# Kernel tuning notes

Measured on AMD Instinct MI355X. Metric: run time of the kernel, lower is better.

Reference implementation:

```python
import jax, jax.numpy as jnp
import numpy as np

B, V, E, D_IN, D_OUT = 8, 10000, 160000, 128, 128
BN_EPS = 1e-5


def setup_inputs() -> dict:
    key = jax.random.key(0)
    ks = jax.random.split(key, 8)
    X = jax.random.normal(ks[0], (B, V, D_IN), dtype=jnp.float32)
    edge_attr = jax.random.normal(ks[1], (B, E), dtype=jnp.float32)
    W_node = jax.random.normal(ks[2], (D_OUT, D_IN), dtype=jnp.float32) * (1.0 / np.sqrt(D_IN))
    W_edge = jax.random.normal(ks[3], (D_OUT, 1), dtype=jnp.float32)
    W_self = jax.random.normal(ks[4], (D_OUT, D_IN), dtype=jnp.float32) * (1.0 / np.sqrt(D_IN))
    b_self = jax.random.normal(ks[5], (D_OUT,), dtype=jnp.float32) * 0.01
    gamma = jnp.ones((D_OUT,), dtype=jnp.float32)
    beta = jnp.zeros((D_OUT,), dtype=jnp.float32)
    edge_index = jax.random.randint(ks[6], (E, 2), 0, V, dtype=jnp.int32)
    return {"X": X, "edge_attr": edge_attr, "W_node": W_node, "W_edge": W_edge,
            "W_self": W_self, "b_self": b_self, "gamma": gamma, "beta": beta,
            "edge_index": edge_index}


def reference(X, edge_attr, W_node, W_edge, W_self, b_self, gamma, beta, edge_index):
    src = edge_index[:, 0]  # [E]
    dst = edge_index[:, 1]  # [E]
    # self-loop linear
    H = jnp.einsum('bvf,of->bvo', X, W_self) + b_self  # [B,V,D_OUT]
    # fused gather -> per-edge message -> scatter-add
    msg = jnp.einsum('bef,of->beo', X[:, src, :], W_node)  # [B,E,D_OUT]
    msg = msg + edge_attr[:, :, None] * W_edge[:, 0][None, None, :]
    aggregated = jnp.zeros_like(H).at[:, dst, :].add(msg)
    H = H + aggregated
    # BatchNorm1d over channel dim (training mode, biased variance over B*V)
    mean = jnp.mean(H, axis=(0, 1))
    var = jnp.var(H, axis=(0, 1))
    Hn = (H - mean) * jax.lax.rsqrt(var + BN_EPS) * gamma + beta
    return jax.nn.relu(Hn)
```

## Files before the change

kernel.cpp:

```cpp
#include <hip/hip_runtime.h>

#define B_ 8
#define V_ 10000
#define E_ 160000
#define DIN 128
#define DOUT 128
#define M_ (B_*V_)
#define NINV (1.0f/80000.0f)
#define BN_EPS 1e-5f

#define GEMM_BLOCKS 625
#define CAP 64

#define WS_CNT     0
#define WS_SUM     10000
#define WS_SUMSQ   10128
#define WS_ZERO_UNITS 10256
#define WS_S       10256
#define WS_SSRC    90256
#define WS_EAS     730256
#define WS_HH      730256
#define WS_WPK     5850256
#define WS_XH      5866640
#define WS_AH      10986640

typedef __attribute__((ext_vector_type(2))) _Float16 half2_t;
typedef __attribute__((ext_vector_type(4))) _Float16 half4_t;
typedef __attribute__((ext_vector_type(8))) _Float16 half8_t;
typedef __attribute__((ext_vector_type(4))) float f32x4;

__device__ inline half2_t i2h(unsigned i) {
    half2_t h; __builtin_memcpy(&h, &i, 4); return h;
}
__device__ inline unsigned h2i(half2_t h) {
    unsigned i; __builtin_memcpy(&i, &h, 4); return i;
}

__global__ __launch_bounds__(256) void prep_kernel(
    const float* __restrict__ X, _Float16* __restrict__ Xh,
    const float* __restrict__ Wself, const float* __restrict__ Wnode,
    _Float16* __restrict__ Wpk,
    const int* __restrict__ EI, const float* __restrict__ EA,
    int* __restrict__ cnt, int* __restrict__ ssrc, float* __restrict__ EAs)
{
    const int blk = blockIdx.x;
    const int t = threadIdx.x;
    if (blk < 10000) {
        int idx = blk * 256 + t;
        float4 v = ((const float4*)X)[idx];
        half4_t o = { (_Float16)v.x, (_Float16)v.y, (_Float16)v.z, (_Float16)v.w };
        ((half4_t*)Xh)[idx] = o;
    } else if (blk < 10016) {
        int g = (blk - 10000) * 256 + t;
        int pair = g >> 6;
        int lane = g & 63;
        int ks = pair >> 3;
        int nt = pair & 7;
        int o = nt * 16 + (lane & 15);
        int k = ks * 32 + (lane >> 4) * 8;
        const float* wsrc = (k < 128) ? (Wself + o * 128 + k)
                                      : (Wnode + o * 128 + (k - 128));
        _Float16* dst = Wpk + ((size_t)pair * 64 + lane) * 8;
#pragma unroll
        for (int j = 0; j < 8; ++j) dst[j] = (_Float16)wsrc[j];
    } else {
        int e = (blk - 10016) * 256 + t;
        int src = EI[2 * e];
        int dst = EI[2 * e + 1];
        int slot = atomicAdd(&cnt[dst], 1);
        if (slot < CAP) {
            int p = dst * CAP + slot;
            ssrc[p] = src;
            float4 v0, v1;
            v0.x = EA[0 * E_ + e]; v0.y = EA[1 * E_ + e];
            v0.z = EA[2 * E_ + e]; v0.w = EA[3 * E_ + e];
            v1.x = EA[4 * E_ + e]; v1.y = EA[5 * E_ + e];
            v1.z = EA[6 * E_ + e]; v1.w = EA[7 * E_ + e];
            *(float4*)(EAs + (size_t)p * 8) = v0;
            *(float4*)(EAs + (size_t)p * 8 + 4) = v1;
        }
    }
}

__global__ __launch_bounds__(256) void gather_kernel(
    const _Float16* __restrict__ Xh, const float* __restrict__ EAs,
    const int* __restrict__ cnt, const int* __restrict__ ssrc,
    _Float16* __restrict__ Ah, float* __restrict__ S)
{
    const int b = blockIdx.x & 7;
    const int dblk = blockIdx.x >> 3;
    const int w = threadIdx.x >> 6;
    const int lane = threadIdx.x & 63;
    const int q = lane >> 4;
    const int sl = lane & 15;
    const int d = dblk * 4 + w;
    const int wid = b * V_ + d;
    const int deg = min(cnt[d], CAP);
    const int k0 = d * CAP;
    const _Float16* Xb = Xh + (size_t)b * V_ * DIN + sl * 8;
    half2_t a0 = (half2_t)0, a1 = (half2_t)0, a2 = (half2_t)0, a3 = (half2_t)0;
    float ea = 0.0f;
    {
        int msrc = 0;
        if (lane < deg) {
            msrc = ssrc[k0 + lane];
            ea = EAs[(size_t)(k0 + lane) * 8 + b];
        }
        int j = 0;
        for (; j + 16 <= deg; j += 16) {
#pragma unroll
            for (int u = 0; u < 4; ++u) {
                int s = __shfl(msrc, j + u * 4 + q);
                uint4 v = *(const uint4*)(Xb + (size_t)s * DIN);
                a0 += i2h(v.x); a1 += i2h(v.y); a2 += i2h(v.z); a3 += i2h(v.w);
            }
        }
        for (; j + 4 <= deg; j += 4) {
            int s = __shfl(msrc, j + q);
            uint4 v = *(const uint4*)(Xb + (size_t)s * DIN);
            a0 += i2h(v.x); a1 += i2h(v.y); a2 += i2h(v.z); a3 += i2h(v.w);
        }
        if (j < deg) {
            int s = __shfl(msrc, j + q);
            if (j + q < deg) {
                uint4 v = *(const uint4*)(Xb + (size_t)s * DIN);
                a0 += i2h(v.x); a1 += i2h(v.y); a2 += i2h(v.z); a3 += i2h(v.w);
            }
        }
    }
#pragma unroll
    for (int off = 32; off >= 16; off >>= 1) {
        a0 += i2h(__shfl_down(h2i(a0), off));
        a1 += i2h(__shfl_down(h2i(a1), off));
        a2 += i2h(__shfl_down(h2i(a2), off));
        a3 += i2h(__shfl_down(h2i(a3), off));
    }
    for (int off = 32; off; off >>= 1) ea += __shfl_down(ea, off);
    if (lane == 0) S[wid] = ea;
    if (lane < 16) {
        uint4 o;
        o.x = h2i(a0); o.y = h2i(a1); o.z = h2i(a2); o.w = h2i(a3);
        *(uint4*)(Ah + (size_t)wid * DIN + sl * 8) = o;
    }
}

__global__ __launch_bounds__(256) void gemm_stats_kernel(
    const _Float16* __restrict__ Xh, const _Float16* __restrict__ Ah,
    const _Float16* __restrict__ Wpk, const float* __restrict__ S,
    const float* __restrict__ bself, const float* __restrict__ wedge,
    _Float16* __restrict__ Hh, float* __restrict__ gsum,
    float* __restrict__ gsumsq)
{
    __shared__ _Float16 wlds[32768];
    __shared__ float cs[128];
    __shared__ float css[128];
    const int t = threadIdx.x;
    const int wave = t >> 6;
    const int lane = t & 63;
    const int quad = lane >> 4;
    const int ln = lane & 15;
    const int rowbase = blockIdx.x * 128 + wave * 32;
    const int m0 = rowbase + ln;
    const int m1 = rowbase + 16 + ln;

#pragma unroll
    for (int i = 0; i < 16; ++i) {
        int chunk = wave * 16 + i;
        __builtin_amdgcn_global_load_lds(
            (const __attribute__((address_space(1))) void*)
                ((const char*)Wpk + (size_t)chunk * 1024 + lane * 16),
            (__attribute__((address_space(3))) void*)
                ((char*)wlds + (size_t)chunk * 1024),
            16, 0, 0);
    }

    if (t < 128) { cs[t] = 0.0f; css[t] = 0.0f; }

    f32x4 acc[2][8];
#pragma unroll
    for (int mt = 0; mt < 2; ++mt)
#pragma unroll
        for (int nt = 0; nt < 8; ++nt) acc[mt][nt] = (f32x4){0.f, 0.f, 0.f, 0.f};

    const _Float16* X0 = Xh + (size_t)m0 * DIN + quad * 8;
    const _Float16* X1 = Xh + (size_t)m1 * DIN + quad * 8;
    const _Float16* A0 = Ah + (size_t)m0 * DIN + quad * 8;
    const _Float16* A1 = Ah + (size_t)m1 * DIN + quad * 8;

    half8_t afr[2][8];
#pragma unroll
    for (int ks = 0; ks < 4; ++ks) {
        afr[0][ks]     = *(const half8_t*)(X0 + ks * 32);
        afr[1][ks]     = *(const half8_t*)(X1 + ks * 32);
        afr[0][4 + ks] = *(const half8_t*)(A0 + ks * 32);
        afr[1][4 + ks] = *(const half8_t*)(A1 + ks * 32);
    }

    __syncthreads();

#pragma unroll
    for (int ks = 0; ks < 8; ++ks) {
#pragma unroll
        for (int nt = 0; nt < 8; ++nt) {
            half8_t bfr = *(const half8_t*)(wlds + (size_t)(ks * 8 + nt) * 512 + lane * 8);
            acc[0][nt] = __builtin_amdgcn_mfma_f32_16x16x32_f16(afr[0][ks], bfr, acc[0][nt], 0, 0, 0);
            acc[1][nt] = __builtin_amdgcn_mfma_f32_16x16x32_f16(afr[1][ks], bfr, acc[1][nt], 0, 0, 0);
        }
    }

    float bs[8], we[8];
#pragma unroll
    for (int nt = 0; nt < 8; ++nt) {
        int c = nt * 16 + ln;
        bs[nt] = bself[c];
        we[nt] = wedge[c];
    }
    float psum[8], psq[8];
#pragma unroll
    for (int nt = 0; nt < 8; ++nt) { psum[nt] = 0.0f; psq[nt] = 0.0f; }

#pragma unroll
    for (int mt = 0; mt < 2; ++mt) {
        const int rbase = rowbase + mt * 16 + quad * 4;
        float sv[4];
#pragma unroll
        for (int r = 0; r < 4; ++r) sv[r] = S[rbase + r];
#pragma unroll
        for (int r = 0; r < 4; ++r) {
            _Float16* Hr = Hh + (size_t)(rbase + r) * DOUT + ln;
#pragma unroll
            for (int nt = 0; nt < 8; ++nt) {
                float h = acc[mt][nt][r] + bs[nt] + sv[r] * we[nt];
                Hr[nt * 16] = (_Float16)h;
                psum[nt] += h;
                psq[nt] += h * h;
            }
        }
    }
#pragma unroll
    for (int nt = 0; nt < 8; ++nt) {
        psum[nt] += __shfl_down(psum[nt], 32);
        psum[nt] += __shfl_down(psum[nt], 16);
        psq[nt] += __shfl_down(psq[nt], 32);
        psq[nt] += __shfl_down(psq[nt], 16);
    }
    __syncthreads();
    if (lane < 16) {
#pragma unroll
        for (int nt = 0; nt < 8; ++nt) {
            atomicAdd(&cs[nt * 16 + ln], psum[nt]);
            atomicAdd(&css[nt * 16 + ln], psq[nt]);
        }
    }
    __syncthreads();
    if (t < 128) atomicAdd(&gsum[t], cs[t]);
    else atomicAdd(&gsumsq[t - 128], css[t - 128]);
}

__global__ __launch_bounds__(256) void norm_relu_kernel(
    const _Float16* __restrict__ Hh, float* __restrict__ H,
    const float* __restrict__ gsum, const float* __restrict__ gsumsq,
    const float* __restrict__ gamma, const float* __restrict__ beta)
{
    const int total = M_ * DOUT / 8;
    for (int idx = blockIdx.x * 256 + threadIdx.x; idx < total;
         idx += gridDim.x * 256) {
        int o8 = (idx & 15) * 8;
        float4 s0 = *(const float4*)(gsum + o8);
        float4 s1 = *(const float4*)(gsum + o8 + 4);
        float4 q0 = *(const float4*)(gsumsq + o8);
        float4 q1 = *(const float4*)(gsumsq + o8 + 4);
        float4 g0 = *(const float4*)(gamma + o8);
        float4 g1 = *(const float4*)(gamma + o8 + 4);
        float4 b0 = *(const float4*)(beta + o8);
        float4 b1 = *(const float4*)(beta + o8 + 4);
        float sc[8], sh[8];
        float sv[8] = {s0.x, s0.y, s0.z, s0.w, s1.x, s1.y, s1.z, s1.w};
        float qv[8] = {q0.x, q0.y, q0.z, q0.w, q1.x, q1.y, q1.z, q1.w};
        float gv[8] = {g0.x, g0.y, g0.z, g0.w, g1.x, g1.y, g1.z, g1.w};
        float bv[8] = {b0.x, b0.y, b0.z, b0.w, b1.x, b1.y, b1.z, b1.w};
#pragma unroll
        for (int j = 0; j < 8; ++j) {
            float mean = sv[j] * NINV;
            float rstd = rsqrtf(qv[j] * NINV - mean * mean + BN_EPS);
            sc[j] = gv[j] * rstd;
            sh[j] = bv[j] - mean * sc[j];
        }
        half8_t hv = ((const half8_t*)Hh)[idx];
        float4 o0, o1;
        o0.x = fmaxf((float)hv[0] * sc[0] + sh[0], 0.0f);
        o0.y = fmaxf((float)hv[1] * sc[1] + sh[1], 0.0f);
        o0.z = fmaxf((float)hv[2] * sc[2] + sh[2], 0.0f);
        o0.w = fmaxf((float)hv[3] * sc[3] + sh[3], 0.0f);
        o1.x = fmaxf((float)hv[4] * sc[4] + sh[4], 0.0f);
        o1.y = fmaxf((float)hv[5] * sc[5] + sh[5], 0.0f);
        o1.z = fmaxf((float)hv[6] * sc[6] + sh[6], 0.0f);
        o1.w = fmaxf((float)hv[7] * sc[7] + sh[7], 0.0f);
        ((float4*)H)[idx * 2]     = o0;
        ((float4*)H)[idx * 2 + 1] = o1;
    }
}

extern "C" void kernel_launch(void* const* d_in, const int* in_sizes, int n_in,
                              void* d_out, int out_size, void* d_ws, size_t ws_size,
                              hipStream_t stream)
{
    const float* X      = (const float*)d_in[0];
    const float* EA     = (const float*)d_in[1];
    const float* Wnode  = (const float*)d_in[2];
    const float* Wedge  = (const float*)d_in[3];
    const float* Wself  = (const float*)d_in[4];
    const float* bself  = (const float*)d_in[5];
    const float* gamma  = (const float*)d_in[6];
    const float* beta   = (const float*)d_in[7];
    const int*   EI     = (const int*)d_in[8];

    int*   wsI    = (int*)d_ws;
    float* wsF    = (float*)d_ws;
    int*   cnt    = wsI + WS_CNT;
    float* gsum   = wsF + WS_SUM;
    float* gsumsq = wsF + WS_SUMSQ;
    float* S      = wsF + WS_S;
    int*   ssrc   = wsI + WS_SSRC;
    float* EAs    = wsF + WS_EAS;
    _Float16* Hh  = (_Float16*)(wsI + WS_HH);
    _Float16* Wpk = (_Float16*)(wsI + WS_WPK);
    _Float16* Xh  = (_Float16*)(wsI + WS_XH);
    _Float16* Ah  = (_Float16*)(wsI + WS_AH);
    float* H      = (float*)d_out;

    hipMemsetAsync(d_ws, 0, (size_t)WS_ZERO_UNITS * 4, stream);

    prep_kernel<<<10641, 256, 0, stream>>>(X, Xh, Wself, Wnode, Wpk, EI, EA,
                                           cnt, ssrc, EAs);

    gather_kernel<<<M_ / 4, 256, 0, stream>>>(Xh, EAs, cnt, ssrc, Ah, S);

    gemm_stats_kernel<<<GEMM_BLOCKS, 256, 0, stream>>>(Xh, Ah, Wpk, S, bself,
                                                       Wedge, Hh, gsum, gsumsq);

    norm_relu_kernel<<<2048, 256, 0, stream>>>(Hh, H, gsum, gsumsq, gamma, beta);
}
```

Baseline: 198.1 us.

## Fuse neighbor gather into GEMM kernel with LDS-staged aggregates and streamed weights

Removes the separate gather kernel and instead has each GEMM wave gather and sum neighbor features for its 32 rows, staging the aggregate in swizzled LDS before the MFMA loop. Weights are streamed into a smaller LDS buffer in four stages, and block IDs are remapped for XCD locality. This avoids writing and re-reading the aggregate matrix and the per-row edge sum through global memory, and saves one launch. In exchange, the gather runs in only 625 blocks with rows processed serially per wave, which cuts the latency-hiding parallelism the standalone gather had.

```diff
diff --git a/kernel.cpp b/kernel.cpp
--- a/kernel.cpp
+++ b/kernel.cpp
@@ -16,13 +16,11 @@
 #define WS_SUM     10000
 #define WS_SUMSQ   10128
 #define WS_ZERO_UNITS 10256
-#define WS_S       10256
-#define WS_SSRC    90256
-#define WS_EAS     730256
-#define WS_HH      730256
-#define WS_WPK     5850256
-#define WS_XH      5866640
-#define WS_AH      10986640
+#define WS_SSRC    10256
+#define WS_EAS     650256
+#define WS_WPK     5770256
+#define WS_XH      5786640
+#define WS_HH      10906640
 
 typedef __attribute__((ext_vector_type(2))) _Float16 half2_t;
 typedef __attribute__((ext_vector_type(4))) _Float16 half4_t;
@@ -82,129 +80,158 @@
     }
 }
 
-__global__ __launch_bounds__(256) void gather_kernel(
-    const _Float16* __restrict__ Xh, const float* __restrict__ EAs,
-    const int* __restrict__ cnt, const int* __restrict__ ssrc,
-    _Float16* __restrict__ Ah, float* __restrict__ S)
+__global__ __launch_bounds__(256, 3) void gemm_fused_kernel(
+    const _Float16* __restrict__ Xh, const _Float16* __restrict__ Wpk,
+    const float* __restrict__ EAs, const int* __restrict__ cnt,
+    const int* __restrict__ ssrc, const float* __restrict__ bself,
+    const float* __restrict__ wedge, _Float16* __restrict__ Hh,
+    float* __restrict__ gsum, float* __restrict__ gsumsq)
 {
-    const int b = blockIdx.x & 7;
-    const int dblk = blockIdx.x >> 3;
-    const int w = threadIdx.x >> 6;
-    const int lane = threadIdx.x & 63;
-    const int q = lane >> 4;
-    const int sl = lane & 15;
-    const int d = dblk * 4 + w;
-    const int wid = b * V_ + d;
-    const int deg = min(cnt[d], CAP);
-    const int k0 = d * CAP;
-    const _Float16* Xb = Xh + (size_t)b * V_ * DIN + sl * 8;
-    half2_t a0 = (half2_t)0, a1 = (half2_t)0, a2 = (half2_t)0, a3 = (half2_t)0;
-    float ea = 0.0f;
-    {
-        int msrc = 0;
-        if (lane < deg) {
-            msrc = ssrc[k0 + lane];
-            ea = EAs[(size_t)(k0 + lane) * 8 + b];
-        }
-        int j = 0;
-        for (; j + 16 <= deg; j += 16) {
-#pragma unroll
-            for (int u = 0; u < 4; ++u) {
-                int s = __shfl(msrc, j + u * 4 + q);
-                uint4 v = *(const uint4*)(Xb + (size_t)s * DIN);
-                a0 += i2h(v.x); a1 += i2h(v.y); a2 += i2h(v.z); a3 += i2h(v.w);
-            }
-        }
-        for (; j + 4 <= deg; j += 4) {
-            int s = __shfl(msrc, j + q);
-            uint4 v = *(const uint4*)(Xb + (size_t)s * DIN);
-            a0 += i2h(v.x); a1 += i2h(v.y); a2 += i2h(v.z); a3 += i2h(v.w);
-        }
-        if (j < deg) {
-            int s = __shfl(msrc, j + q);
-            if (j + q < deg) {
-                uint4 v = *(const uint4*)(Xb + (size_t)s * DIN);
-                a0 += i2h(v.x); a1 += i2h(v.y); a2 += i2h(v.z); a3 += i2h(v.w);
-            }
-        }
-    }
-#pragma unroll
-    for (int off = 32; off >= 16; off >>= 1) {
-        a0 += i2h(__shfl_down(h2i(a0), off));
-        a1 += i2h(__shfl_down(h2i(a1), off));
-        a2 += i2h(__shfl_down(h2i(a2), off));
-        a3 += i2h(__shfl_down(h2i(a3), off));
-    }
-    for (int off = 32; off; off >>= 1) ea += __shfl_down(ea, off);
-    if (lane == 0) S[wid] = ea;
-    if (lane < 16) {
-        uint4 o;
-        o.x = h2i(a0); o.y = h2i(a1); o.z = h2i(a2); o.w = h2i(a3);
-        *(uint4*)(Ah + (size_t)wid * DIN + sl * 8) = o;
-    }
-}
-
-__global__ __launch_bounds__(256) void gemm_stats_kernel(
-    const _Float16* __restrict__ Xh, const _Float16* __restrict__ Ah,
-    const _Float16* __restrict__ Wpk, const float* __restrict__ S,
-    const float* __restrict__ bself, const float* __restrict__ wedge,
-    _Float16* __restrict__ Hh, float* __restrict__ gsum,
-    float* __restrict__ gsumsq)
-{
-    __shared__ _Float16 wlds[32768];
-    __shared__ float cs[128];
-    __shared__ float css[128];
+    __shared__ _Float16 wlds[8192];
+    __shared__ _Float16 agg[16384];
+    float* cs  = (float*)agg;
+    float* css = ((float*)agg) + 128;
+
     const int t = threadIdx.x;
+    const int orig = blockIdx.x;
+    const int xcd = orig & 7, off = orig >> 3;
+    const int qq = GEMM_BLOCKS >> 3, rr = GEMM_BLOCKS & 7;
+    const int bid = (xcd < rr ? xcd * (qq + 1)
+                              : rr * (qq + 1) + (xcd - rr) * qq) + off;
+
     const int wave = t >> 6;
     const int lane = t & 63;
     const int quad = lane >> 4;
     const int ln = lane & 15;
-    const int rowbase = blockIdx.x * 128 + wave * 32;
-    const int m0 = rowbase + ln;
-    const int m1 = rowbase + 16 + ln;
-
-#pragma unroll
-    for (int i = 0; i < 16; ++i) {
-        int chunk = wave * 16 + i;
+    const int rowbase = bid * 128 + wave * 32;
+
+#pragma unroll
+    for (int i = 0; i < 4; ++i) {
+        int lc = wave * 4 + i;
         __builtin_amdgcn_global_load_lds(
             (const __attribute__((address_space(1))) void*)
-                ((const char*)Wpk + (size_t)chunk * 1024 + lane * 16),
+                ((const char*)Wpk + (size_t)lc * 1024 + lane * 16),
             (__attribute__((address_space(3))) void*)
-                ((char*)wlds + (size_t)chunk * 1024),
+                ((char*)wlds + (size_t)lc * 1024),
             16, 0, 0);
     }
 
-    if (t < 128) { cs[t] = 0.0f; css[t] = 0.0f; }
-
-    f32x4 acc[2][8];
-#pragma unroll
-    for (int mt = 0; mt < 2; ++mt)
-#pragma unroll
-        for (int nt = 0; nt < 8; ++nt) acc[mt][nt] = (f32x4){0.f, 0.f, 0.f, 0.f};
-
+    float sv[2][4];
+    for (int r = 0; r < 32; ++r) {
+        int lrow = wave * 32 + r;
+        int m = bid * 128 + lrow;
+        int b = m / V_;
+        int d = m - b * V_;
+        int deg = min(cnt[d], CAP);
+        int k0 = d * CAP;
+        const _Float16* Xb = Xh + (size_t)b * V_ * DIN + ln * 8;
+        half2_t a0 = (half2_t)0, a1 = (half2_t)0, a2 = (half2_t)0, a3 = (half2_t)0;
+        int msrc = 0; float ea = 0.0f;
+        if (lane < deg) {
+            msrc = ssrc[k0 + lane];
+            ea = EAs[(size_t)(k0 + lane) * 8 + b];
+        }
+        int j = 0;
+        for (; j + 16 <= deg; j += 16) {
+#pragma unroll
+            for (int u = 0; u < 4; ++u) {
+                int s = __shfl(msrc, j + u * 4 + quad);
+                uint4 v = *(const uint4*)(Xb + (size_t)s * DIN);
+                a0 += i2h(v.x); a1 += i2h(v.y); a2 += i2h(v.z); a3 += i2h(v.w);
+            }
+        }
+        for (; j + 4 <= deg; j += 4) {
+            int s = __shfl(msrc, j + quad);
+            uint4 v = *(const uint4*)(Xb + (size_t)s * DIN);
+            a0 += i2h(v.x); a1 += i2h(v.y); a2 += i2h(v.z); a3 += i2h(v.w);
+        }
+        if (j < deg) {
+            int s = __shfl(msrc, j + quad);
+            if (j + quad < deg) {
+                uint4 v = *(const uint4*)(Xb + (size_t)s * DIN);
+                a0 += i2h(v.x); a1 += i2h(v.y); a2 += i2h(v.z); a3 += i2h(v.w);
+            }
+        }
+#pragma unroll
+        for (int off2 = 32; off2 >= 16; off2 >>= 1) {
+            a0 += i2h(__shfl_down(h2i(a0), off2));
+            a1 += i2h(__shfl_down(h2i(a1), off2));
+            a2 += i2h(__shfl_down(h2i(a2), off2));
+            a3 += i2h(__shfl_down(h2i(a3), off2));
+        }
+        for (int off2 = 32; off2; off2 >>= 1) ea += __shfl_down(ea, off2);
+        float ea_r = __shfl(ea, 0);
+#pragma unroll
+        for (int mt = 0; mt < 2; ++mt)
+#pragma unroll
+            for (int r2 = 0; r2 < 4; ++r2)
+                if (r == mt * 16 + quad * 4 + r2) sv[mt][r2] = ea_r;
+        if (lane < 16) {
+            uint4 o; o.x = h2i(a0); o.y = h2i(a1); o.z = h2i(a2); o.w = h2i(a3);
+            int slot = lrow * 16 + (ln ^ (lrow & 7));
+            *(uint4*)((char*)agg + (size_t)slot * 16) = o;
+        }
+    }
+
+    half8_t agr0[4], agr1[4];
+    {
+        const int R0 = wave * 32 + ln;
+        const int R1 = R0 + 16;
+#pragma unroll
+        for (int ks2 = 0; ks2 < 4; ++ks2) {
+            int sl0 = R0 * 16 + ((ks2 * 4 + quad) ^ (R0 & 7));
+            int sl1 = R1 * 16 + ((ks2 * 4 + quad) ^ (R1 & 7));
+            agr0[ks2] = *(const half8_t*)((const char*)agg + (size_t)sl0 * 16);
+            agr1[ks2] = *(const half8_t*)((const char*)agg + (size_t)sl1 * 16);
+        }
+    }
+
+    const int m0 = rowbase + ln, m1 = rowbase + 16 + ln;
     const _Float16* X0 = Xh + (size_t)m0 * DIN + quad * 8;
     const _Float16* X1 = Xh + (size_t)m1 * DIN + quad * 8;
-    const _Float16* A0 = Ah + (size_t)m0 * DIN + quad * 8;
-    const _Float16* A1 = Ah + (size_t)m1 * DIN + quad * 8;
-
-    half8_t afr[2][8];
+    half8_t afr0[4], afr1[4];
 #pragma unroll
     for (int ks = 0; ks < 4; ++ks) {
-        afr[0][ks]     = *(const half8_t*)(X0 + ks * 32);
-        afr[1][ks]     = *(const half8_t*)(X1 + ks * 32);
-        afr[0][4 + ks] = *(const half8_t*)(A0 + ks * 32);
-        afr[1][4 + ks] = *(const half8_t*)(A1 + ks * 32);
-    }
+        afr0[ks] = *(const half8_t*)(X0 + ks * 32);
+        afr1[ks] = *(const half8_t*)(X1 + ks * 32);
+    }
+
+    f32x4 acc[2][8];
+#pragma unroll
+    for (int mt = 0; mt < 2; ++mt)
+#pragma unroll
+        for (int nt = 0; nt < 8; ++nt) acc[mt][nt] = (f32x4){0.f, 0.f, 0.f, 0.f};
 
     __syncthreads();
-
-#pragma unroll
-    for (int ks = 0; ks < 8; ++ks) {
-#pragma unroll
-        for (int nt = 0; nt < 8; ++nt) {
-            half8_t bfr = *(const half8_t*)(wlds + (size_t)(ks * 8 + nt) * 512 + lane * 8);
-            acc[0][nt] = __builtin_amdgcn_mfma_f32_16x16x32_f16(afr[0][ks], bfr, acc[0][nt], 0, 0, 0);
-            acc[1][nt] = __builtin_amdgcn_mfma_f32_16x16x32_f16(afr[1][ks], bfr, acc[1][nt], 0, 0, 0);
+    if (t < 128) { cs[t] = 0.0f; css[t] = 0.0f; }
+
+#pragma unroll
+    for (int s = 0; s < 4; ++s) {
+#pragma unroll
+        for (int ksl = 0; ksl < 2; ++ksl) {
+            const int kg = s * 2 + ksl;
+            half8_t af0 = (kg < 4) ? afr0[kg] : agr0[kg - 4];
+            half8_t af1 = (kg < 4) ? afr1[kg] : agr1[kg - 4];
+#pragma unroll
+            for (int nt = 0; nt < 8; ++nt) {
+                half8_t bfr = *(const half8_t*)(wlds + (size_t)(ksl * 8 + nt) * 512 + lane * 8);
+                acc[0][nt] = __builtin_amdgcn_mfma_f32_16x16x32_f16(af0, bfr, acc[0][nt], 0, 0, 0);
+                acc[1][nt] = __builtin_amdgcn_mfma_f32_16x16x32_f16(af1, bfr, acc[1][nt], 0, 0, 0);
+            }
+        }
+        if (s < 3) {
+            __syncthreads();
+#pragma unroll
+            for (int i = 0; i < 4; ++i) {
+                int lc = wave * 4 + i;
+                __builtin_amdgcn_global_load_lds(
+                    (const __attribute__((address_space(1))) void*)
+                        ((const char*)Wpk + (size_t)((s + 1) * 16 + lc) * 1024 + lane * 16),
+                    (__attribute__((address_space(3))) void*)
+                        ((char*)wlds + (size_t)lc * 1024),
+                    16, 0, 0);
+            }
+            __syncthreads();
         }
     }
 
@@ -221,16 +248,13 @@
 
 #pragma unroll
     for (int mt = 0; mt < 2; ++mt) {
-        const int rbase = rowbase + mt * 16 + quad * 4;
-        float sv[4];
-#pragma unroll
-        for (int r = 0; r < 4; ++r) sv[r] = S[rbase + r];
-#pragma unroll
-        for (int r = 0; r < 4; ++r) {
-            _Float16* Hr = Hh + (size_t)(rbase + r) * DOUT + ln;
+        const int rbl = wave * 32 + mt * 16 + quad * 4;
+#pragma unroll
+        for (int r2 = 0; r2 < 4; ++r2) {
+            _Float16* Hr = Hh + (size_t)(bid * 128 + rbl + r2) * DOUT + ln;
 #pragma unroll
             for (int nt = 0; nt < 8; ++nt) {
-                float h = acc[mt][nt][r] + bs[nt] + sv[r] * we[nt];
+                float h = acc[mt][nt][r2] + bs[nt] + sv[mt][r2] * we[nt];
                 Hr[nt * 16] = (_Float16)h;
                 psum[nt] += h;
                 psq[nt] += h * h;
@@ -241,8 +265,8 @@
     for (int nt = 0; nt < 8; ++nt) {
         psum[nt] += __shfl_down(psum[nt], 32);
         psum[nt] += __shfl_down(psum[nt], 16);
-        psq[nt] += __shfl_down(psq[nt], 32);
-        psq[nt] += __shfl_down(psq[nt], 16);
+        psq[nt]  += __shfl_down(psq[nt], 32);
+        psq[nt]  += __shfl_down(psq[nt], 16);
     }
     __syncthreads();
     if (lane < 16) {
@@ -275,13 +299,13 @@
         float4 b0 = *(const float4*)(beta + o8);
         float4 b1 = *(const float4*)(beta + o8 + 4);
         float sc[8], sh[8];
-        float sv[8] = {s0.x, s0.y, s0.z, s0.w, s1.x, s1.y, s1.z, s1.w};
+        float svv[8] = {s0.x, s0.y, s0.z, s0.w, s1.x, s1.y, s1.z, s1.w};
         float qv[8] = {q0.x, q0.y, q0.z, q0.w, q1.x, q1.y, q1.z, q1.w};
         float gv[8] = {g0.x, g0.y, g0.z, g0.w, g1.x, g1.y, g1.z, g1.w};
         float bv[8] = {b0.x, b0.y, b0.z, b0.w, b1.x, b1.y, b1.z, b1.w};
 #pragma unroll
         for (int j = 0; j < 8; ++j) {
-            float mean = sv[j] * NINV;
+            float mean = svv[j] * NINV;
             float rstd = rsqrtf(qv[j] * NINV - mean * mean + BN_EPS);
             sc[j] = gv[j] * rstd;
             sh[j] = bv[j] - mean * sc[j];
@@ -320,13 +344,11 @@
     int*   cnt    = wsI + WS_CNT;
     float* gsum   = wsF + WS_SUM;
     float* gsumsq = wsF + WS_SUMSQ;
-    float* S      = wsF + WS_S;
     int*   ssrc   = wsI + WS_SSRC;
     float* EAs    = wsF + WS_EAS;
-    _Float16* Hh  = (_Float16*)(wsI + WS_HH);
     _Float16* Wpk = (_Float16*)(wsI + WS_WPK);
     _Float16* Xh  = (_Float16*)(wsI + WS_XH);
-    _Float16* Ah  = (_Float16*)(wsI + WS_AH);
+    _Float16* Hh  = (_Float16*)(wsI + WS_HH);
     float* H      = (float*)d_out;
 
     hipMemsetAsync(d_ws, 0, (size_t)WS_ZERO_UNITS * 4, stream);
@@ -334,10 +356,9 @@
     prep_kernel<<<10641, 256, 0, stream>>>(X, Xh, Wself, Wnode, Wpk, EI, EA,
                                            cnt, ssrc, EAs);
 
-    gather_kernel<<<M_ / 4, 256, 0, stream>>>(Xh, EAs, cnt, ssrc, Ah, S);
-
-    gemm_stats_kernel<<<GEMM_BLOCKS, 256, 0, stream>>>(Xh, Ah, Wpk, S, bself,
-                                                       Wedge, Hh, gsum, gsumsq);
+    gemm_fused_kernel<<<GEMM_BLOCKS, 256, 0, stream>>>(Xh, Wpk, EAs, cnt, ssrc,
+                                                       bself, Wedge, Hh,
+                                                       gsum, gsumsq);
 
     norm_relu_kernel<<<2048, 256, 0, stream>>>(Hh, H, gsum, gsumsq, gamma, beta);
 }
```

New measurement: 216.2 us. 9.2% more time.

## Split GEMM waves across output columns with register-resident weights, drop LDS staging

Applied to the files above, without the earlier changes.

The GEMM+stats kernel now gives each wave a 32-column slice of the output for all 128 rows of the block. Weights are loaded straight into registers instead of being staged through 64KB of LDS. Per-block stat reduction through shared memory is replaced by direct global atomics, and launch bounds request 2 blocks per SM. This removes the LDS footprint and barriers, but every wave now re-reads the full A tile (X and aggregated rows) from global/L2, the global atomic count rises, and register pressure grows.

```diff
diff --git a/kernel.cpp b/kernel.cpp
--- a/kernel.cpp
+++ b/kernel.cpp
@@ -144,117 +144,94 @@
     }
 }
 
-__global__ __launch_bounds__(256) void gemm_stats_kernel(
+__global__ __launch_bounds__(256, 2) void gemm_stats_kernel(
     const _Float16* __restrict__ Xh, const _Float16* __restrict__ Ah,
     const _Float16* __restrict__ Wpk, const float* __restrict__ S,
     const float* __restrict__ bself, const float* __restrict__ wedge,
     _Float16* __restrict__ Hh, float* __restrict__ gsum,
     float* __restrict__ gsumsq)
 {
-    __shared__ _Float16 wlds[32768];
-    __shared__ float cs[128];
-    __shared__ float css[128];
     const int t = threadIdx.x;
     const int wave = t >> 6;
     const int lane = t & 63;
     const int quad = lane >> 4;
     const int ln = lane & 15;
-    const int rowbase = blockIdx.x * 128 + wave * 32;
-    const int m0 = rowbase + ln;
-    const int m1 = rowbase + 16 + ln;
-
-#pragma unroll
-    for (int i = 0; i < 16; ++i) {
-        int chunk = wave * 16 + i;
-        __builtin_amdgcn_global_load_lds(
-            (const __attribute__((address_space(1))) void*)
-                ((const char*)Wpk + (size_t)chunk * 1024 + lane * 16),
-            (__attribute__((address_space(3))) void*)
-                ((char*)wlds + (size_t)chunk * 1024),
-            16, 0, 0);
-    }
-
-    if (t < 128) { cs[t] = 0.0f; css[t] = 0.0f; }
-
-    f32x4 acc[2][8];
-#pragma unroll
-    for (int mt = 0; mt < 2; ++mt)
-#pragma unroll
-        for (int nt = 0; nt < 8; ++nt) acc[mt][nt] = (f32x4){0.f, 0.f, 0.f, 0.f};
-
-    const _Float16* X0 = Xh + (size_t)m0 * DIN + quad * 8;
-    const _Float16* X1 = Xh + (size_t)m1 * DIN + quad * 8;
-    const _Float16* A0 = Ah + (size_t)m0 * DIN + quad * 8;
-    const _Float16* A1 = Ah + (size_t)m1 * DIN + quad * 8;
-
-    half8_t afr[2][8];
-#pragma unroll
-    for (int ks = 0; ks < 4; ++ks) {
-        afr[0][ks]     = *(const half8_t*)(X0 + ks * 32);
-        afr[1][ks]     = *(const half8_t*)(X1 + ks * 32);
-        afr[0][4 + ks] = *(const half8_t*)(A0 + ks * 32);
-        afr[1][4 + ks] = *(const half8_t*)(A1 + ks * 32);
-    }
-
-    __syncthreads();
+    const int bid = blockIdx.x;
+    const int rowbase = bid * 128;
+
+    half8_t bfr[8][2];
+#pragma unroll
+    for (int ks = 0; ks < 8; ++ks)
+#pragma unroll
+        for (int ntl = 0; ntl < 2; ++ntl)
+            bfr[ks][ntl] = *(const half8_t*)(
+                Wpk + ((size_t)(ks * 8 + wave * 2 + ntl) * 64 + lane) * 8);
+
+    f32x4 acc[8][2];
+#pragma unroll
+    for (int mt = 0; mt < 8; ++mt)
+#pragma unroll
+        for (int ntl = 0; ntl < 2; ++ntl) acc[mt][ntl] = (f32x4){0.f,0.f,0.f,0.f};
+
+    const _Float16* Xr = Xh + (size_t)(rowbase + ln) * DIN + quad * 8;
+    const _Float16* Ar = Ah + (size_t)(rowbase + ln) * DIN + quad * 8;
 
 #pragma unroll
     for (int ks = 0; ks < 8; ++ks) {
-#pragma unroll
-        for (int nt = 0; nt < 8; ++nt) {
-            half8_t bfr = *(const half8_t*)(wlds + (size_t)(ks * 8 + nt) * 512 + lane * 8);
-            acc[0][nt] = __builtin_amdgcn_mfma_f32_16x16x32_f16(afr[0][ks], bfr, acc[0][nt], 0, 0, 0);
-            acc[1][nt] = __builtin_amdgcn_mfma_f32_16x16x32_f16(afr[1][ks], bfr, acc[1][nt], 0, 0, 0);
-        }
-    }
-
-    float bs[8], we[8];
-#pragma unroll
-    for (int nt = 0; nt < 8; ++nt) {
-        int c = nt * 16 + ln;
-        bs[nt] = bself[c];
-        we[nt] = wedge[c];
-    }
-    float psum[8], psq[8];
-#pragma unroll
-    for (int nt = 0; nt < 8; ++nt) { psum[nt] = 0.0f; psq[nt] = 0.0f; }
-
-#pragma unroll
-    for (int mt = 0; mt < 2; ++mt) {
-        const int rbase = rowbase + mt * 16 + quad * 4;
+        const _Float16* base = (ks < 4) ? (Xr + ks * 32) : (Ar + (ks - 4) * 32);
+        half8_t af[8];
+#pragma unroll
+        for (int mt = 0; mt < 8; ++mt)
+            af[mt] = *(const half8_t*)(base + (size_t)mt * 16 * DIN);
+#pragma unroll
+        for (int mt = 0; mt < 8; ++mt) {
+            acc[mt][0] = __builtin_amdgcn_mfma_f32_16x16x32_f16(af[mt], bfr[ks][0], acc[mt][0], 0, 0, 0);
+            acc[mt][1] = __builtin_amdgcn_mfma_f32_16x16x32_f16(af[mt], bfr[ks][1], acc[mt][1], 0, 0, 0);
+        }
+    }
+
+    float bs[2], we[2];
+#pragma unroll
+    for (int ntl = 0; ntl < 2; ++ntl) {
+        int c = wave * 32 + ntl * 16 + ln;
+        bs[ntl] = bself[c];
+        we[ntl] = wedge[c];
+    }
+    float psum[2] = {0.f, 0.f}, psq[2] = {0.f, 0.f};
+
+#pragma unroll
+    for (int mt = 0; mt < 8; ++mt) {
+        const int rb = rowbase + mt * 16 + quad * 4;
         float sv[4];
 #pragma unroll
-        for (int r = 0; r < 4; ++r) sv[r] = S[rbase + r];
+        for (int r = 0; r < 4; ++r) sv[r] = S[rb + r];
 #pragma unroll
         for (int r = 0; r < 4; ++r) {
-            _Float16* Hr = Hh + (size_t)(rbase + r) * DOUT + ln;
-#pragma unroll
-            for (int nt = 0; nt < 8; ++nt) {
-                float h = acc[mt][nt][r] + bs[nt] + sv[r] * we[nt];
-                Hr[nt * 16] = (_Float16)h;
-                psum[nt] += h;
-                psq[nt] += h * h;
+            _Float16* Hr = Hh + (size_t)(rb + r) * DOUT + wave * 32 + ln;
+#pragma unroll
+            for (int ntl = 0; ntl < 2; ++ntl) {
+                float h = acc[mt][ntl][r] + bs[ntl] + sv[r] * we[ntl];
+                Hr[ntl * 16] = (_Float16)h;
+                psum[ntl] += h;
+                psq[ntl] += h * h;
             }
         }
     }
 #pragma unroll
-    for (int nt = 0; nt < 8; ++nt) {
-        psum[nt] += __shfl_down(psum[nt], 32);
-        psum[nt] += __shfl_down(psum[nt], 16);
-        psq[nt] += __shfl_down(psq[nt], 32);
-        psq[nt] += __shfl_down(psq[nt], 16);
-    }
-    __syncthreads();
+    for (int ntl = 0; ntl < 2; ++ntl) {
+        psum[ntl] += __shfl_down(psum[ntl], 32);
+        psum[ntl] += __shfl_down(psum[ntl], 16);
+        psq[ntl]  += __shfl_down(psq[ntl], 32);
+        psq[ntl]  += __shfl_down(psq[ntl], 16);
+    }
     if (lane < 16) {
 #pragma unroll
-        for (int nt = 0; nt < 8; ++nt) {
-            atomicAdd(&cs[nt * 16 + ln], psum[nt]);
-            atomicAdd(&css[nt * 16 + ln], psq[nt]);
-        }
-    }
-    __syncthreads();
-    if (t < 128) atomicAdd(&gsum[t], cs[t]);
-    else atomicAdd(&gsumsq[t - 128], css[t - 128]);
+        for (int ntl = 0; ntl < 2; ++ntl) {
+            int c = wave * 32 + ntl * 16 + lane;
+            atomicAdd(&gsum[c], psum[ntl]);
+            atomicAdd(&gsumsq[c], psq[ntl]);
+        }
+    }
 }
 
 __global__ __launch_bounds__(256) void norm_relu_kernel(
@@ -275,13 +252,13 @@
         float4 b0 = *(const float4*)(beta + o8);
         float4 b1 = *(const float4*)(beta + o8 + 4);
         float sc[8], sh[8];
-        float sv[8] = {s0.x, s0.y, s0.z, s0.w, s1.x, s1.y, s1.z, s1.w};
+        float svv[8] = {s0.x, s0.y, s0.z, s0.w, s1.x, s1.y, s1.z, s1.w};
         float qv[8] = {q0.x, q0.y, q0.z, q0.w, q1.x, q1.y, q1.z, q1.w};
         float gv[8] = {g0.x, g0.y, g0.z, g0.w, g1.x, g1.y, g1.z, g1.w};
         float bv[8] = {b0.x, b0.y, b0.z, b0.w, b1.x, b1.y, b1.z, b1.w};
 #pragma unroll
         for (int j = 0; j < 8; ++j) {
-            float mean = sv[j] * NINV;
+            float mean = svv[j] * NINV;
             float rstd = rsqrtf(qv[j] * NINV - mean * mean + BN_EPS);
             sc[j] = gv[j] * rstd;
             sh[j] = bv[j] - mean * sc[j];
```

Result: slower. 203.2 us (+2.6%).
